# Kernel tuning notes

Measured on AMD Instinct MI355X. Metric: run time of the kernel, lower is better.

Reference implementation:

```python
import jax, jax.numpy as jnp
import numpy as np

B = 32768
NM = 3      # number of modalities (len(mk))
NE = 8      # number of experts
D_IN = 768
D_P = 128   # per-modality projection dim
D_X = D_P * NM  # 384, concatenated feature dim


def setup_inputs() -> dict:
    key = jax.random.key(0)
    ks = jax.random.split(key, 16)
    s = 0.02
    return {
        "feat_text": jax.random.normal(ks[0], (B, D_IN), jnp.float32),
        "feat_audio": jax.random.normal(ks[1], (B, D_IN), jnp.float32),
        "feat_video": jax.random.normal(ks[2], (B, D_IN), jnp.float32),
        "proj_w": jax.random.normal(ks[3], (NM, D_IN, D_P), jnp.float32) * s,
        "proj_b": jax.random.normal(ks[4], (NM, D_P), jnp.float32) * s,
        "exp_w1": jax.random.normal(ks[5], (NE, D_X, D_P), jnp.float32) * s,
        "exp_b1": jax.random.normal(ks[6], (NE, D_P), jnp.float32) * s,
        "exp_w2": jax.random.normal(ks[7], (NE, D_P, D_P), jnp.float32) * s,
        "exp_b2": jax.random.normal(ks[8], (NE, D_P), jnp.float32) * s,
        "gate_w": jax.random.normal(ks[9], (D_X, NE), jnp.float32) * s,
        "gate_b": jax.random.normal(ks[10], (NE,), jnp.float32) * s,
        "pre_w": jax.random.normal(ks[11], (D_P, 64), jnp.float32) * s,
        "pre_b": jax.random.normal(ks[12], (64,), jnp.float32) * s,
        "head_w": jax.random.normal(ks[13], (64, 2), jnp.float32) * s,
        "head_b": jax.random.normal(ks[14], (2,), jnp.float32) * s,
    }


def reference(feat_text, feat_audio, feat_video, proj_w, proj_b,
              exp_w1, exp_b1, exp_w2, exp_b2, gate_w, gate_b,
              pre_w, pre_b, head_w, head_b):
    feats = jnp.stack([feat_text, feat_audio, feat_video], axis=0)  # [M,B,768]
    # per-modality projections, then concat: [B, 128*M]
    proj = jnp.einsum('mbd,mdp->mbp', feats, proj_w) + proj_b[:, None, :]
    x = jnp.concatenate(jnp.split(proj, NM, axis=0), axis=-1)[0]  # [B, 384]
    # gate: softmax over 8 experts
    gw = jax.nn.softmax(x @ gate_w + gate_b, axis=-1)  # [B, 8]
    # all experts as batched GEMM: [E,B,128]
    h = jax.nn.relu(jnp.einsum('bx,exh->ebh', x, exp_w1) + exp_b1[:, None, :])
    eo = jnp.einsum('ebh,eho->ebo', h, exp_w2) + exp_b2[:, None, :]
    fused = jnp.einsum('be,ebh->bh', gw, eo)  # weighted sum over experts
    penult = jax.nn.relu(fused @ pre_w + pre_b)  # Dropout is identity in eval
    logits = penult @ head_w + head_b  # [B, 2]
    return logits
```

## Files before the change

### kernel.cpp

```cpp
#include <hip/hip_runtime.h>
#include <hip/hip_bf16.h>

#define B_ROWS 32768

typedef unsigned short u16;
typedef unsigned int u32;
typedef float f32x4 __attribute__((ext_vector_type(4)));
typedef __bf16 bf16x8 __attribute__((ext_vector_type(8)));

__device__ __forceinline__ u16 f2bf(float f){
    union { float f; u32 u; } v; v.f = f;
    return (u16)((v.u + 0x7FFFu + ((v.u >> 16) & 1u)) >> 16);
}
__device__ __forceinline__ float bf2f(u16 h){
    union { u32 u; float f; } v; v.u = ((u32)h) << 16; return v.f;
}
__device__ __forceinline__ u32 cvtpk(float lo, float hi){
    u32 r;
    asm("v_cvt_pk_bf16_f32 %0, %1, %2" : "=v"(r) : "v"(lo), "v"(hi));
    return r;
}
__device__ __forceinline__ void async_cp16(void* lds_dst, const void* g_src){
    __builtin_amdgcn_global_load_lds(
        (const __attribute__((address_space(1))) unsigned int*)g_src,
        (__attribute__((address_space(3))) unsigned int*)lds_dst, 16, 0, 0);
}

__global__ void cast_weights_kernel(const float* __restrict__ proj_w,
                                    const float* __restrict__ exp_w1,
                                    const float* __restrict__ exp_w2,
                                    const float* __restrict__ pre_w,
                                    const float* __restrict__ gate_w,
                                    u16* __restrict__ pimg, u16* __restrict__ w1img,
                                    u16* __restrict__ w2img, u16* __restrict__ prwT,
                                    u16* __restrict__ gwimg){
    int i = blockIdx.x * 256 + threadIdx.x;
    if (i < 294912){
        int m = i / 98304, r = i % 98304;
        int c = r / 4096, rr = r % 4096;
        int col = rr >> 5, kk = rr & 31;
        int kb = kk ^ (((col >> 1) & 3) << 3);
        pimg[i] = f2bf(proj_w[m*98304 + (c*32 + kb)*128 + col]);
    } else if (i < 688128){
        int j = i - 294912;
        int e = j / 49152, r = j % 49152;
        int ph = r / 4096, rr = r % 4096;
        int q = rr >> 10, col = (rr >> 3) & 127, el = rr & 7;
        w1img[j] = f2bf(exp_w1[e*49152 + (ph*32 + q*8 + el)*128 + col]);
    } else if (i < 819200){
        int j = i - 688128;
        int e = j / 16384, r = j % 16384;
        int c2 = r / 4096, rr = r % 4096;
        int q = rr >> 10, col = (rr >> 3) & 127, el = rr & 7;
        w2img[j] = f2bf(exp_w2[e*16384 + (c2*32 + q*8 + el)*128 + col]);
    } else if (i < 827392){
        int j = i - 819200;
        int o = j / 128, k = j % 128;
        prwT[j] = f2bf(pre_w[k*64 + o]);
    } else if (i < 833536){
        int j = i - 827392;
        int e = j / 384, k = j % 384;
        gwimg[j] = (e < 8) ? f2bf(gate_w[k*8 + e]) : (u16)0;
    }
}

#define XS_OFF   0
#define A_OFF    98304
#define B_OFF    147456
#define HS_OFF   98304
#define GWT_OFF  131072
#define B1_OFF   135168
#define B2_OFF   137216
#define WB_OFF   139264

__global__ __launch_bounds__(512, 2) void fused_kernel(
    const float* __restrict__ ft, const float* __restrict__ fa, const float* __restrict__ fv,
    const u16* __restrict__ pimg, const float* __restrict__ proj_b,
    const u16* __restrict__ w1img, const u16* __restrict__ w2img,
    const u16* __restrict__ prwT, const u16* __restrict__ gwimg,
    const float* __restrict__ gate_b, const float* __restrict__ exp_b1, const float* __restrict__ exp_b2,
    const float* __restrict__ pre_b, const float* __restrict__ head_w, const float* __restrict__ head_b,
    float* __restrict__ out)
{
    __shared__ __align__(16) char lds[163840];
    const int tid = threadIdx.x;
    const int lane = tid & 63, wid = tid >> 6;
    const int wr = wid >> 1, wc = wid & 1;
    const int lr = lane & 15, q = lane >> 4;
    const int blk = blockIdx.x;
    const int row0 = blk * 128;
    const char* w1b = (const char*)w1img;
    const char* w2b = (const char*)w2img;
    char* HsB = lds + HS_OFF;
    u16* b1L = (u16*)(lds + B1_OFF);
    u16* b2L = (u16*)(lds + B2_OFF);

    float pb0[4], pb1[4], pb2[4];
    #pragma unroll
    for (int ni = 0; ni < 4; ni++){
        int c = wc*64 + ni*16 + lr;
        pb0[ni] = proj_b[c];
        pb1[ni] = proj_b[128 + c];
        pb2[ni] = proj_b[256 + c];
    }
    asm volatile("s_waitcnt vmcnt(0)" ::: "memory");

    u32 aoffs[2];
    #pragma unroll
    for (int i = 0; i < 2; i++){
        int P = i*8192 + tid*16;
        int row = P >> 7, inner = P & 127;
        aoffs[i] = (u32)((row0 + row)*3072 + (inner ^ ((row & 7) << 4)));
    }

#define ASTAGE(c) do{                                                          \
        int mm_ = (c) / 24, kk_ = (c) % 24;                                    \
        const char* ab_ = (const char*)(mm_ == 0 ? ft : mm_ == 1 ? fa : fv);   \
        char* la_ = lds + A_OFF + ((c) % 3)*16384 + tid*16;                    \
        async_cp16(la_,        ab_ + aoffs[0] + kk_*128);                      \
        async_cp16(la_ + 8192, ab_ + aoffs[1] + kk_*128);                      \
    }while(0)

#define BSTAGE(c) do{                                                          \
        int mm_ = (c) / 24, kk_ = (c) % 24;                                    \
        async_cp16(lds + B_OFF + ((c) % 2)*8192 + tid*16,                      \
                   (const char*)pimg + mm_*196608 + kk_*8192 + tid*16);        \
    }while(0)

#define PCONSUME(c) do{                                                        \
        const char* Abuf = lds + A_OFF + ((c) % 3)*16384;                      \
        const char* Bbuf = lds + B_OFF + ((c) % 2)*8192;                       \
        bf16x8 af[2];                                                          \
        _Pragma("unroll")                                                      \
        for (int mi = 0; mi < 2; mi++){                                        \
            int row = wr*32 + mi*16 + lr;                                      \
            int aoff = row*128 + ((q*32) ^ ((row & 7) << 4));                  \
            f32x4 a0 = *(const f32x4*)(Abuf + aoff);                           \
            f32x4 a1 = *(const f32x4*)(Abuf + (aoff ^ 16));                    \
            union { u32 w[4]; bf16x8 v; } u;                                   \
            u.w[0] = cvtpk(a0.x, a0.y); u.w[1] = cvtpk(a0.z, a0.w);            \
            u.w[2] = cvtpk(a1.x, a1.y); u.w[3] = cvtpk(a1.z, a1.w);            \
            af[mi] = u.v;                                                      \
        }                                                                      \
        _Pragma("unroll")                                                      \
        for (int ni = 0; ni < 4; ni++){                                        \
            int col = wc*64 + ni*16 + lr;                                      \
            int boff = col*64 + ((q*16) ^ (((col >> 1) & 3) << 4));            \
            bf16x8 bf = *(const bf16x8*)(Bbuf + boff);                         \
            acc[0][ni] = __builtin_amdgcn_mfma_f32_16x16x32_bf16(af[0], bf, acc[0][ni], 0, 0, 0); \
            acc[1][ni] = __builtin_amdgcn_mfma_f32_16x16x32_bf16(af[1], bf, acc[1][ni], 0, 0, 0); \
        }                                                                      \
    }while(0)

#define PHASE_A_MOD(MC, PB) do{                                                \
        _Pragma("unroll 1")                                                    \
        for (int kt = 0; kt < 24; kt++){                                       \
            int t = MC*24 + kt;                                                \
            __builtin_amdgcn_sched_barrier(0);                                 \
            __builtin_amdgcn_s_barrier();                                      \
            if (t < 71) BSTAGE(t + 1);                                         \
            if (t < 70) ASTAGE(t + 2);                                         \
            if (t < 70)       asm volatile("s_waitcnt vmcnt(5)" ::: "memory"); \
            else if (t == 70) asm volatile("s_waitcnt vmcnt(3)" ::: "memory"); \
            else              asm volatile("s_waitcnt vmcnt(0)" ::: "memory"); \
            __builtin_amdgcn_s_barrier();                                      \
            __builtin_amdgcn_sched_barrier(0);                                 \
            PCONSUME(t);                                                       \
        }                                                                      \
        _Pragma("unroll")                                                      \
        for (int mi = 0; mi < 2; mi++)                                         \
            _Pragma("unroll")                                                  \
            for (int ni = 0; ni < 4; ni++){                                    \
                int lcol = wc*64 + ni*16 + lr;                                 \
                int colg = MC*128 + lcol;                                      \
                int ktI = colg >> 5, qI = (colg >> 3) & 3, el = colg & 7;      \
                _Pragma("unroll")                                              \
                for (int j = 0; j < 4; j++){                                   \
                    int row = wr*32 + mi*16 + q*4 + j;                         \
                    *(u16*)(lds + (row >> 6)*49152 + ktI*4096 + qI*1024        \
                            + (row & 63)*16 + el*2) = f2bf(acc[mi][ni][j] + PB[ni]); \
                    acc[mi][ni][j] = 0.f;                                      \
                }                                                              \
            }                                                                  \
    }while(0)

    f32x4 acc[2][4];
    #pragma unroll
    for (int i = 0; i < 2; i++)
        #pragma unroll
        for (int j = 0; j < 4; j++) acc[i][j] = {0.f, 0.f, 0.f, 0.f};

    BSTAGE(0); ASTAGE(0); ASTAGE(1);
    PHASE_A_MOD(0, pb0);
    PHASE_A_MOD(1, pb1);
    PHASE_A_MOD(2, pb2);
#undef ASTAGE
#undef BSTAGE
#undef PCONSUME
#undef PHASE_A_MOD

    asm volatile("s_waitcnt lgkmcnt(0)" ::: "memory");
    __builtin_amdgcn_sched_barrier(0);
    __builtin_amdgcn_s_barrier();

    {
        const char* src = w1b + tid*16;
        async_cp16(lds + WB_OFF + 0*8192 + tid*16, src);
        async_cp16(lds + WB_OFF + 1*8192 + tid*16, src + 8192);
        async_cp16(lds + WB_OFF + 2*8192 + tid*16, src + 16384);
    }
    for (int i = tid; i < 1024; i += 512){
        b1L[i] = f2bf(exp_b1[i]);
        b2L[i] = f2bf(exp_b2[i]);
    }
    {
        f32x4 ga = {0.f, 0.f, 0.f, 0.f};
        const char* xb = lds + (wid >> 2)*49152 + ((wid & 3)*16 + lr)*16 + q*1024;
        const u16* gwp = gwimg + lr*384 + q*8;
        #pragma unroll
        for (int kt = 0; kt < 12; kt++){
            bf16x8 af = *(const bf16x8*)(xb + kt*4096);
            bf16x8 gb = *(const bf16x8*)(gwp + kt*32);
            ga = __builtin_amdgcn_mfma_f32_16x16x32_bf16(af, gb, ga, 0, 0, 0);
        }
        float gbv = gate_b[lr & 7];
        float gw4[4];
        #pragma unroll
        for (int j = 0; j < 4; j++){
            float v = ga[j] + gbv;
            float mx = v;
            mx = fmaxf(mx, __shfl_xor(mx, 1));
            mx = fmaxf(mx, __shfl_xor(mx, 2));
            mx = fmaxf(mx, __shfl_xor(mx, 4));
            float s = __expf(v - mx);
            float t = s;
            t += __shfl_xor(t, 1);
            t += __shfl_xor(t, 2);
            t += __shfl_xor(t, 4);
            gw4[j] = s / t;
        }
        if (lr < 8){
            f32x4 wv = {gw4[0], gw4[1], gw4[2], gw4[3]};
            *(f32x4*)(lds + GWT_OFF + lr*512 + (wid*16 + q*4)*4) = wv;
        }
    }
    asm volatile("s_waitcnt vmcnt(0) lgkmcnt(0)" ::: "memory");
    __builtin_amdgcn_sched_barrier(0);
    __builtin_amdgcn_s_barrier();

#define WGROUP_STAGE(gg2) do{                                                  \
        int e2_ = (gg2) / 6, i2_ = (gg2) % 6;                                  \
        if (i2_ < 4){                                                          \
            const char* src_ = w1b + e2_*98304 + i2_*3*8192 + tid*16;          \
            async_cp16(lds + WB_OFF + 0*8192 + tid*16, src_);                  \
            async_cp16(lds + WB_OFF + 1*8192 + tid*16, src_ + 8192);           \
            async_cp16(lds + WB_OFF + 2*8192 + tid*16, src_ + 16384);          \
        } else {                                                               \
            const char* src_ = w2b + e2_*32768 + (i2_ - 4)*2*8192 + tid*16;    \
            async_cp16(lds + WB_OFF + 0*8192 + tid*16, src_);                  \
            async_cp16(lds + WB_OFF + 1*8192 + tid*16, src_ + 8192);           \
        }                                                                      \
    }while(0)

    f32x4 fus[2][4];
    #pragma unroll
    for (int i = 0; i < 2; i++)
        #pragma unroll
        for (int j = 0; j < 4; j++) fus[i][j] = {0.f, 0.f, 0.f, 0.f};

    #pragma unroll 1
    for (int e = 0; e < 8; e++){
        f32x4 ac1[2][4];
        #pragma unroll
        for (int i = 0; i < 2; i++)
            #pragma unroll
            for (int j = 0; j < 4; j++) ac1[i][j] = {0.f, 0.f, 0.f, 0.f};

        #pragma unroll 1
        for (int grp = 0; grp < 4; grp++){
            #pragma unroll
            for (int c = 0; c < 3; c++){
                int ph = grp*3 + c;
                const char* wsl = lds + WB_OFF + c*8192 + q*2048;
                const char* xa  = lds + (wr >> 1)*49152 + ph*4096 + q*1024;
                bf16x8 af0 = *(const bf16x8*)(xa + ((wr & 1)*32 + lr)*16);
                bf16x8 af1 = *(const bf16x8*)(xa + ((wr & 1)*32 + 16 + lr)*16);
                #pragma unroll
                for (int ni = 0; ni < 4; ni++){
                    bf16x8 bf = *(const bf16x8*)(wsl + (wc*64 + ni*16 + lr)*16);
                    ac1[0][ni] = __builtin_amdgcn_mfma_f32_16x16x32_bf16(af0, bf, ac1[0][ni], 0, 0, 0);
                    ac1[1][ni] = __builtin_amdgcn_mfma_f32_16x16x32_bf16(af1, bf, ac1[1][ni], 0, 0, 0);
                }
            }
            if (grp == 3){
                #pragma unroll
                for (int mi = 0; mi < 2; mi++)
                    #pragma unroll
                    for (int ni = 0; ni < 4; ni++){
                        int col = wc*64 + ni*16 + lr;
                        float b1v = bf2f(b1L[e*128 + col]);
                        #pragma unroll
                        for (int j = 0; j < 4; j++){
                            int row = wr*32 + mi*16 + q*4 + j;
                            *(u16*)(HsB + row*256 + ((col*2) ^ ((row & 7) << 4)))
                                = f2bf(fmaxf(ac1[mi][ni][j] + b1v, 0.f));
                        }
                    }
                asm volatile("s_waitcnt lgkmcnt(0)" ::: "memory");
            }
            __builtin_amdgcn_sched_barrier(0);
            __builtin_amdgcn_s_barrier();
            WGROUP_STAGE(e*6 + grp + 1);
            asm volatile("s_waitcnt vmcnt(0)" ::: "memory");
            __builtin_amdgcn_s_barrier();
            __builtin_amdgcn_sched_barrier(0);
        }

        f32x4 ac2[2][4];
        #pragma unroll
        for (int i = 0; i < 2; i++)
            #pragma unroll
            for (int j = 0; j < 4; j++) ac2[i][j] = {0.f, 0.f, 0.f, 0.f};

        #pragma unroll 1
        for (int grp = 0; grp < 2; grp++){
            #pragma unroll
            for (int c = 0; c < 2; c++){
                int p2 = grp*2 + c;
                const char* wsl = lds + WB_OFF + c*8192 + q*2048;
                int cb = p2*64 + q*16;
                int rowA = wr*32 + lr;
                int rowB = wr*32 + 16 + lr;
                bf16x8 af0 = *(const bf16x8*)(HsB + rowA*256 + (cb ^ ((rowA & 7) << 4)));
                bf16x8 af1 = *(const bf16x8*)(HsB + rowB*256 + (cb ^ ((rowB & 7) << 4)));
                #pragma unroll
                for (int ni = 0; ni < 4; ni++){
                    bf16x8 bf = *(const bf16x8*)(wsl + (wc*64 + ni*16 + lr)*16);
                    ac2[0][ni] = __builtin_amdgcn_mfma_f32_16x16x32_bf16(af0, bf, ac2[0][ni], 0, 0, 0);
                    ac2[1][ni] = __builtin_amdgcn_mfma_f32_16x16x32_bf16(af1, bf, ac2[1][ni], 0, 0, 0);
                }
            }
            int gg2 = e*6 + 5 + grp;
            __builtin_amdgcn_sched_barrier(0);
            __builtin_amdgcn_s_barrier();
            if (gg2 < 48){
                WGROUP_STAGE(gg2);
                asm volatile("s_waitcnt vmcnt(0)" ::: "memory");
            }
            __builtin_amdgcn_s_barrier();
            __builtin_amdgcn_sched_barrier(0);
        }
        #pragma unroll
        for (int mi = 0; mi < 2; mi++){
            f32x4 gwv = *(const f32x4*)(lds + GWT_OFF + e*512 + (wr*32 + mi*16 + q*4)*4);
            #pragma unroll
            for (int ni = 0; ni < 4; ni++){
                int col = wc*64 + ni*16 + lr;
                float b2v = bf2f(b2L[e*128 + col]);
                #pragma unroll
                for (int j = 0; j < 4; j++)
                    fus[mi][ni][j] += gwv[j] * (ac2[mi][ni][j] + b2v);
            }
        }
    }
#undef WGROUP_STAGE

    __builtin_amdgcn_sched_barrier(0);
    __builtin_amdgcn_s_barrier();
    #pragma unroll
    for (int mi = 0; mi < 2; mi++)
        #pragma unroll
        for (int ni = 0; ni < 4; ni++){
            int col = wc*64 + ni*16 + lr;
            #pragma unroll
            for (int j = 0; j < 4; j++){
                int row = wr*32 + mi*16 + q*4 + j;
                *(u16*)(HsB + row*256 + ((col*2) ^ ((row & 7) << 4))) = f2bf(fus[mi][ni][j]);
            }
        }
    asm volatile("s_waitcnt lgkmcnt(0)" ::: "memory");
    __builtin_amdgcn_sched_barrier(0);
    __builtin_amdgcn_s_barrier();

    f32x4 ap[4];
    #pragma unroll
    for (int i = 0; i < 4; i++) ap[i] = {0.f, 0.f, 0.f, 0.f};
    #pragma unroll
    for (int kt = 0; kt < 4; kt++){
        int row = wid*16 + lr;
        int cb = kt*64 + q*16;
        bf16x8 af = *(const bf16x8*)(HsB + row*256 + (cb ^ ((row & 7) << 4)));
        #pragma unroll
        for (int ni = 0; ni < 4; ni++){
            bf16x8 bf = *(const bf16x8*)(prwT + (size_t)(ni*16 + lr)*128 + kt*32 + q*8);
            ap[ni] = __builtin_amdgcn_mfma_f32_16x16x32_bf16(af, bf, ap[ni], 0, 0, 0);
        }
    }
    float* Pen = (float*)lds;
    #pragma unroll
    for (int ni = 0; ni < 4; ni++){
        int col = ni*16 + lr;
        float pbv = pre_b[col];
        #pragma unroll
        for (int j = 0; j < 4; j++){
            int row = wid*16 + q*4 + j;
            Pen[row*68 + col] = fmaxf(ap[ni][j] + pbv, 0.f);
        }
    }
    asm volatile("s_waitcnt lgkmcnt(0)" ::: "memory");
    __builtin_amdgcn_sched_barrier(0);
    __builtin_amdgcn_s_barrier();
    if (tid < 256){
        int r = tid >> 1, c = tid & 1;
        float s = head_b[c];
        #pragma unroll 8
        for (int k = 0; k < 64; k++) s += Pen[r*68 + k] * head_w[k*2 + c];
        out[(size_t)(blk*128 + r)*2 + c] = s;
    }
}

extern "C" void kernel_launch(void* const* d_in, const int* in_sizes, int n_in,
                              void* d_out, int out_size, void* d_ws, size_t ws_size,
                              hipStream_t stream) {
    const float* ft     = (const float*)d_in[0];
    const float* fa     = (const float*)d_in[1];
    const float* fv     = (const float*)d_in[2];
    const float* proj_w = (const float*)d_in[3];
    const float* proj_b = (const float*)d_in[4];
    const float* exp_w1 = (const float*)d_in[5];
    const float* exp_b1 = (const float*)d_in[6];
    const float* exp_w2 = (const float*)d_in[7];
    const float* exp_b2 = (const float*)d_in[8];
    const float* gate_w = (const float*)d_in[9];
    const float* gate_b = (const float*)d_in[10];
    const float* pre_w  = (const float*)d_in[11];
    const float* pre_b  = (const float*)d_in[12];
    const float* head_w = (const float*)d_in[13];
    const float* head_b = (const float*)d_in[14];
    float* out = (float*)d_out;

    u16* pimg  = (u16*)d_ws;
    u16* w1img = pimg + 294912;
    u16* w2img = w1img + 393216;
    u16* prwT  = w2img + 131072;
    u16* gwimg = prwT + 8192;

    cast_weights_kernel<<<3256, 256, 0, stream>>>(proj_w, exp_w1, exp_w2, pre_w, gate_w,
                                                  pimg, w1img, w2img, prwT, gwimg);
    fused_kernel<<<256, 512, 0, stream>>>(ft, fa, fv, pimg, proj_b,
                                          w1img, w2img, prwT, gwimg,
                                          gate_b, exp_b1, exp_b2,
                                          pre_b, head_w, head_b, out);
}
```

Before: 120.9 us.

## Halve workgroup to 4 waves, each wave computing a 64x64 tile

The fused kernel now runs 256 threads (4 waves) per block instead of 512. Each wave owns a 64-row by 64-column output tile with 4x4 MFMA accumulators instead of 2x4, and all staging loops, waitcnt counts and epilogues are rescaled to match. The goal is to reuse each B fragment across more MFMAs, cut LDS reads per flop and lower barrier overhead. In exchange it roughly doubles accumulator register pressure and halves the wave count that hides load latency, while the same 256 blocks and LDS footprint are kept.

After: 136.2 us. +12.7%, slower.

```diff
diff --git a/kernel.cpp b/kernel.cpp
--- a/kernel.cpp
+++ b/kernel.cpp
@@ -73,7 +73,7 @@
 #define B2_OFF   137216
 #define WB_OFF   139264
 
-__global__ __launch_bounds__(512, 2) void fused_kernel(
+__global__ __launch_bounds__(256, 1) void fused_kernel(
     const float* __restrict__ ft, const float* __restrict__ fa, const float* __restrict__ fv,
     const u16* __restrict__ pimg, const float* __restrict__ proj_b,
     const u16* __restrict__ w1img, const u16* __restrict__ w2img,
@@ -105,10 +105,10 @@
     }
     asm volatile("s_waitcnt vmcnt(0)" ::: "memory");
 
-    u32 aoffs[2];
-    #pragma unroll
-    for (int i = 0; i < 2; i++){
-        int P = i*8192 + tid*16;
+    u32 aoffs[4];
+    #pragma unroll
+    for (int i = 0; i < 4; i++){
+        int P = i*4096 + tid*16;
         int row = P >> 7, inner = P & 127;
         aoffs[i] = (u32)((row0 + row)*3072 + (inner ^ ((row & 7) << 4)));
     }
@@ -117,23 +117,27 @@
         int mm_ = (c) / 24, kk_ = (c) % 24;                                    \
         const char* ab_ = (const char*)(mm_ == 0 ? ft : mm_ == 1 ? fa : fv);   \
         char* la_ = lds + A_OFF + ((c) % 3)*16384 + tid*16;                    \
-        async_cp16(la_,        ab_ + aoffs[0] + kk_*128);                      \
-        async_cp16(la_ + 8192, ab_ + aoffs[1] + kk_*128);                      \
+        async_cp16(la_,         ab_ + aoffs[0] + kk_*128);                     \
+        async_cp16(la_ + 4096,  ab_ + aoffs[1] + kk_*128);                     \
+        async_cp16(la_ + 8192,  ab_ + aoffs[2] + kk_*128);                     \
+        async_cp16(la_ + 12288, ab_ + aoffs[3] + kk_*128);                     \
     }while(0)
 
 #define BSTAGE(c) do{                                                          \
         int mm_ = (c) / 24, kk_ = (c) % 24;                                    \
-        async_cp16(lds + B_OFF + ((c) % 2)*8192 + tid*16,                      \
-                   (const char*)pimg + mm_*196608 + kk_*8192 + tid*16);        \
+        const char* gb_ = (const char*)pimg + mm_*196608 + kk_*8192 + tid*16;  \
+        char* lb_ = lds + B_OFF + ((c) % 2)*8192 + tid*16;                     \
+        async_cp16(lb_,        gb_);                                           \
+        async_cp16(lb_ + 4096, gb_ + 4096);                                    \
     }while(0)
 
 #define PCONSUME(c) do{                                                        \
         const char* Abuf = lds + A_OFF + ((c) % 3)*16384;                      \
         const char* Bbuf = lds + B_OFF + ((c) % 2)*8192;                       \
-        bf16x8 af[2];                                                          \
+        bf16x8 af[4];                                                          \
         _Pragma("unroll")                                                      \
-        for (int mi = 0; mi < 2; mi++){                                        \
-            int row = wr*32 + mi*16 + lr;                                      \
+        for (int mi = 0; mi < 4; mi++){                                        \
+            int row = wr*64 + mi*16 + lr;                                      \
             int aoff = row*128 + ((q*32) ^ ((row & 7) << 4));                  \
             f32x4 a0 = *(const f32x4*)(Abuf + aoff);                           \
             f32x4 a1 = *(const f32x4*)(Abuf + (aoff ^ 16));                    \
@@ -147,8 +151,9 @@
             int col = wc*64 + ni*16 + lr;                                      \
             int boff = col*64 + ((q*16) ^ (((col >> 1) & 3) << 4));            \
             bf16x8 bf = *(const bf16x8*)(Bbuf + boff);                         \
-            acc[0][ni] = __builtin_amdgcn_mfma_f32_16x16x32_bf16(af[0], bf, acc[0][ni], 0, 0, 0); \
-            acc[1][ni] = __builtin_amdgcn_mfma_f32_16x16x32_bf16(af[1], bf, acc[1][ni], 0, 0, 0); \
+            _Pragma("unroll")                                                  \
+            for (int mi = 0; mi < 4; mi++)                                     \
+                acc[mi][ni] = __builtin_amdgcn_mfma_f32_16x16x32_bf16(af[mi], bf, acc[mi][ni], 0, 0, 0); \
         }                                                                      \
     }while(0)
 
@@ -160,15 +165,15 @@
             __builtin_amdgcn_s_barrier();                                      \
             if (t < 71) BSTAGE(t + 1);                                         \
             if (t < 70) ASTAGE(t + 2);                                         \
-            if (t < 70)       asm volatile("s_waitcnt vmcnt(5)" ::: "memory"); \
-            else if (t == 70) asm volatile("s_waitcnt vmcnt(3)" ::: "memory"); \
+            if (t < 70)       asm volatile("s_waitcnt vmcnt(10)" ::: "memory"); \
+            else if (t == 70) asm volatile("s_waitcnt vmcnt(6)" ::: "memory"); \
             else              asm volatile("s_waitcnt vmcnt(0)" ::: "memory"); \
             __builtin_amdgcn_s_barrier();                                      \
             __builtin_amdgcn_sched_barrier(0);                                 \
             PCONSUME(t);                                                       \
         }                                                                      \
         _Pragma("unroll")                                                      \
-        for (int mi = 0; mi < 2; mi++)                                         \
+        for (int mi = 0; mi < 4; mi++)                                         \
             _Pragma("unroll")                                                  \
             for (int ni = 0; ni < 4; ni++){                                    \
                 int lcol = wc*64 + ni*16 + lr;                                 \
@@ -176,7 +181,7 @@
                 int ktI = colg >> 5, qI = (colg >> 3) & 3, el = colg & 7;      \
                 _Pragma("unroll")                                              \
                 for (int j = 0; j < 4; j++){                                   \
-                    int row = wr*32 + mi*16 + q*4 + j;                         \
+                    int row = wr*64 + mi*16 + q*4 + j;                         \
                     *(u16*)(lds + (row >> 6)*49152 + ktI*4096 + qI*1024        \
                             + (row & 63)*16 + el*2) = f2bf(acc[mi][ni][j] + PB[ni]); \
                     acc[mi][ni][j] = 0.f;                                      \
@@ -184,9 +189,9 @@
             }                                                                  \
     }while(0)
 
-    f32x4 acc[2][4];
-    #pragma unroll
-    for (int i = 0; i < 2; i++)
+    f32x4 acc[4][4];
+    #pragma unroll
+    for (int i = 0; i < 4; i++)
         #pragma unroll
         for (int j = 0; j < 4; j++) acc[i][j] = {0.f, 0.f, 0.f, 0.f};
 
@@ -205,17 +210,21 @@
 
     {
         const char* src = w1b + tid*16;
-        async_cp16(lds + WB_OFF + 0*8192 + tid*16, src);
-        async_cp16(lds + WB_OFF + 1*8192 + tid*16, src + 8192);
-        async_cp16(lds + WB_OFF + 2*8192 + tid*16, src + 16384);
-    }
-    for (int i = tid; i < 1024; i += 512){
+        #pragma unroll
+        for (int s = 0; s < 3; s++){
+            async_cp16(lds + WB_OFF + s*8192 + tid*16,        src + s*8192);
+            async_cp16(lds + WB_OFF + s*8192 + tid*16 + 4096, src + s*8192 + 4096);
+        }
+    }
+    for (int i = tid; i < 1024; i += 256){
         b1L[i] = f2bf(exp_b1[i]);
         b2L[i] = f2bf(exp_b2[i]);
     }
-    {
+    #pragma unroll
+    for (int hr = 0; hr < 2; hr++){
+        int g16 = wid*2 + hr;
         f32x4 ga = {0.f, 0.f, 0.f, 0.f};
-        const char* xb = lds + (wid >> 2)*49152 + ((wid & 3)*16 + lr)*16 + q*1024;
+        const char* xb = lds + (g16 >> 2)*49152 + ((g16 & 3)*16 + lr)*16 + q*1024;
         const u16* gwp = gwimg + lr*384 + q*8;
         #pragma unroll
         for (int kt = 0; kt < 12; kt++){
@@ -241,7 +250,7 @@
         }
         if (lr < 8){
             f32x4 wv = {gw4[0], gw4[1], gw4[2], gw4[3]};
-            *(f32x4*)(lds + GWT_OFF + lr*512 + (wid*16 + q*4)*4) = wv;
+            *(f32x4*)(lds + GWT_OFF + lr*512 + (g16*16 + q*4)*4) = wv;
         }
     }
     asm volatile("s_waitcnt vmcnt(0) lgkmcnt(0)" ::: "memory");
@@ -251,28 +260,33 @@
 #define WGROUP_STAGE(gg2) do{                                                  \
         int e2_ = (gg2) / 6, i2_ = (gg2) % 6;                                  \
         if (i2_ < 4){                                                          \
-            const char* src_ = w1b + e2_*98304 + i2_*3*8192 + tid*16;          \
-            async_cp16(lds + WB_OFF + 0*8192 + tid*16, src_);                  \
-            async_cp16(lds + WB_OFF + 1*8192 + tid*16, src_ + 8192);           \
-            async_cp16(lds + WB_OFF + 2*8192 + tid*16, src_ + 16384);          \
+            const char* src_ = w1b + e2_*98304 + i2_*24576 + tid*16;           \
+            _Pragma("unroll")                                                  \
+            for (int s = 0; s < 3; s++){                                       \
+                async_cp16(lds + WB_OFF + s*8192 + tid*16,        src_ + s*8192);        \
+                async_cp16(lds + WB_OFF + s*8192 + tid*16 + 4096, src_ + s*8192 + 4096); \
+            }                                                                  \
         } else {                                                               \
-            const char* src_ = w2b + e2_*32768 + (i2_ - 4)*2*8192 + tid*16;    \
-            async_cp16(lds + WB_OFF + 0*8192 + tid*16, src_);                  \
-            async_cp16(lds + WB_OFF + 1*8192 + tid*16, src_ + 8192);           \
+            const char* src_ = w2b + e2_*32768 + (i2_ - 4)*16384 + tid*16;     \
+            _Pragma("unroll")                                                  \
+            for (int s = 0; s < 2; s++){                                       \
+                async_cp16(lds + WB_OFF + s*8192 + tid*16,        src_ + s*8192);        \
+                async_cp16(lds + WB_OFF + s*8192 + tid*16 + 4096, src_ + s*8192 + 4096); \
+            }                                                                  \
         }                                                                      \
     }while(0)
 
-    f32x4 fus[2][4];
-    #pragma unroll
-    for (int i = 0; i < 2; i++)
+    f32x4 fus[4][4];
+    #pragma unroll
+    for (int i = 0; i < 4; i++)
         #pragma unroll
         for (int j = 0; j < 4; j++) fus[i][j] = {0.f, 0.f, 0.f, 0.f};
 
     #pragma unroll 1
     for (int e = 0; e < 8; e++){
-        f32x4 ac1[2][4];
-        #pragma unroll
-        for (int i = 0; i < 2; i++)
+        f32x4 ac1[4][4];
+        #pragma unroll
+        for (int i = 0; i < 4; i++)
             #pragma unroll
             for (int j = 0; j < 4; j++) ac1[i][j] = {0.f, 0.f, 0.f, 0.f};
 
@@ -282,26 +296,29 @@
             for (int c = 0; c < 3; c++){
                 int ph = grp*3 + c;
                 const char* wsl = lds + WB_OFF + c*8192 + q*2048;
-                const char* xa  = lds + (wr >> 1)*49152 + ph*4096 + q*1024;
-                bf16x8 af0 = *(const bf16x8*)(xa + ((wr & 1)*32 + lr)*16);
-                bf16x8 af1 = *(const bf16x8*)(xa + ((wr & 1)*32 + 16 + lr)*16);
+                const char* xa  = lds + wr*49152 + ph*4096 + q*1024;
+                bf16x8 af[4];
+                #pragma unroll
+                for (int mi = 0; mi < 4; mi++)
+                    af[mi] = *(const bf16x8*)(xa + (mi*16 + lr)*16);
                 #pragma unroll
                 for (int ni = 0; ni < 4; ni++){
                     bf16x8 bf = *(const bf16x8*)(wsl + (wc*64 + ni*16 + lr)*16);
-                    ac1[0][ni] = __builtin_amdgcn_mfma_f32_16x16x32_bf16(af0, bf, ac1[0][ni], 0, 0, 0);
-                    ac1[1][ni] = __builtin_amdgcn_mfma_f32_16x16x32_bf16(af1, bf, ac1[1][ni], 0, 0, 0);
+                    #pragma unroll
+                    for (int mi = 0; mi < 4; mi++)
+                        ac1[mi][ni] = __builtin_amdgcn_mfma_f32_16x16x32_bf16(af[mi], bf, ac1[mi][ni], 0, 0, 0);
                 }
             }
             if (grp == 3){
                 #pragma unroll
-                for (int mi = 0; mi < 2; mi++)
+                for (int mi = 0; mi < 4; mi++)
                     #pragma unroll
                     for (int ni = 0; ni < 4; ni++){
                         int col = wc*64 + ni*16 + lr;
                         float b1v = bf2f(b1L[e*128 + col]);
                         #pragma unroll
                         for (int j = 0; j < 4; j++){
-                            int row = wr*32 + mi*16 + q*4 + j;
+                            int row = wr*64 + mi*16 + q*4 + j;
                             *(u16*)(HsB + row*256 + ((col*2) ^ ((row & 7) << 4)))
                                 = f2bf(fmaxf(ac1[mi][ni][j] + b1v, 0.f));
                         }
@@ -316,9 +333,9 @@
             __builtin_amdgcn_sched_barrier(0);
         }
 
-        f32x4 ac2[2][4];
-        #pragma unroll
-        for (int i = 0; i < 2; i++)
+        f32x4 ac2[4][4];
+        #pragma unroll
+        for (int i = 0; i < 4; i++)
             #pragma unroll
             for (int j = 0; j < 4; j++) ac2[i][j] = {0.f, 0.f, 0.f, 0.f};
 
@@ -329,15 +346,18 @@
                 int p2 = grp*2 + c;
                 const char* wsl = lds + WB_OFF + c*8192 + q*2048;
                 int cb = p2*64 + q*16;
-                int rowA = wr*32 + lr;
-                int rowB = wr*32 + 16 + lr;
-                bf16x8 af0 = *(const bf16x8*)(HsB + rowA*256 + (cb ^ ((rowA & 7) << 4)));
-                bf16x8 af1 = *(const bf16x8*)(HsB + rowB*256 + (cb ^ ((rowB & 7) << 4)));
+                bf16x8 af[4];
+                #pragma unroll
+                for (int mi = 0; mi < 4; mi++){
+                    int rowA = wr*64 + mi*16 + lr;
+                    af[mi] = *(const bf16x8*)(HsB + rowA*256 + (cb ^ ((rowA & 7) << 4)));
+                }
                 #pragma unroll
                 for (int ni = 0; ni < 4; ni++){
                     bf16x8 bf = *(const bf16x8*)(wsl + (wc*64 + ni*16 + lr)*16);
-                    ac2[0][ni] = __builtin_amdgcn_mfma_f32_16x16x32_bf16(af0, bf, ac2[0][ni], 0, 0, 0);
-                    ac2[1][ni] = __builtin_amdgcn_mfma_f32_16x16x32_bf16(af1, bf, ac2[1][ni], 0, 0, 0);
+                    #pragma unroll
+                    for (int mi = 0; mi < 4; mi++)
+                        ac2[mi][ni] = __builtin_amdgcn_mfma_f32_16x16x32_bf16(af[mi], bf, ac2[mi][ni], 0, 0, 0);
                 }
             }
             int gg2 = e*6 + 5 + grp;
@@ -351,8 +371,8 @@
             __builtin_amdgcn_sched_barrier(0);
         }
         #pragma unroll
-        for (int mi = 0; mi < 2; mi++){
-            f32x4 gwv = *(const f32x4*)(lds + GWT_OFF + e*512 + (wr*32 + mi*16 + q*4)*4);
+        for (int mi = 0; mi < 4; mi++){
+            f32x4 gwv = *(const f32x4*)(lds + GWT_OFF + e*512 + (wr*64 + mi*16 + q*4)*4);
             #pragma unroll
             for (int ni = 0; ni < 4; ni++){
                 int col = wc*64 + ni*16 + lr;
@@ -368,13 +388,13 @@
     __builtin_amdgcn_sched_barrier(0);
     __builtin_amdgcn_s_barrier();
     #pragma unroll
-    for (int mi = 0; mi < 2; mi++)
+    for (int mi = 0; mi < 4; mi++)
         #pragma unroll
         for (int ni = 0; ni < 4; ni++){
             int col = wc*64 + ni*16 + lr;
             #pragma unroll
             for (int j = 0; j < 4; j++){
-                int row = wr*32 + mi*16 + q*4 + j;
+                int row = wr*64 + mi*16 + q*4 + j;
                 *(u16*)(HsB + row*256 + ((col*2) ^ ((row & 7) << 4))) = f2bf(fus[mi][ni][j]);
             }
         }
@@ -382,35 +402,42 @@
     __builtin_amdgcn_sched_barrier(0);
     __builtin_amdgcn_s_barrier();
 
-    f32x4 ap[4];
-    #pragma unroll
-    for (int i = 0; i < 4; i++) ap[i] = {0.f, 0.f, 0.f, 0.f};
+    f32x4 ap[2][4];
+    #pragma unroll
+    for (int i = 0; i < 2; i++)
+        #pragma unroll
+        for (int j = 0; j < 4; j++) ap[i][j] = {0.f, 0.f, 0.f, 0.f};
     #pragma unroll
     for (int kt = 0; kt < 4; kt++){
-        int row = wid*16 + lr;
         int cb = kt*64 + q*16;
-        bf16x8 af = *(const bf16x8*)(HsB + row*256 + (cb ^ ((row & 7) << 4)));
+        #pragma unroll
+        for (int mi = 0; mi < 2; mi++){
+            int row = wid*32 + mi*16 + lr;
+            bf16x8 af = *(const bf16x8*)(HsB + row*256 + (cb ^ ((row & 7) << 4)));
+            #pragma unroll
+            for (int ni = 0; ni < 4; ni++){
+                bf16x8 bf = *(const bf16x8*)(prwT + (size_t)(ni*16 + lr)*128 + kt*32 + q*8);
+                ap[mi][ni] = __builtin_amdgcn_mfma_f32_16x16x32_bf16(af, bf, ap[mi][ni], 0, 0, 0);
+            }
+        }
+    }
+    float* Pen = (float*)lds;
+    #pragma unroll
+    for (int mi = 0; mi < 2; mi++)
         #pragma unroll
         for (int ni = 0; ni < 4; ni++){
-            bf16x8 bf = *(const bf16x8*)(prwT + (size_t)(ni*16 + lr)*128 + kt*32 + q*8);
-            ap[ni] = __builtin_amdgcn_mfma_f32_16x16x32_bf16(af, bf, ap[ni], 0, 0, 0);
-        }
-    }
-    float* Pen = (float*)lds;
-    #pragma unroll
-    for (int ni = 0; ni < 4; ni++){
-        int col = ni*16 + lr;
-        float pbv = pre_b[col];
-        #pragma unroll
-        for (int j = 0; j < 4; j++){
-            int row = wid*16 + q*4 + j;
-            Pen[row*68 + col] = fmaxf(ap[ni][j] + pbv, 0.f);
-        }
-    }
+            int col = ni*16 + lr;
+            float pbv = pre_b[col];
+            #pragma unroll
+            for (int j = 0; j < 4; j++){
+                int row = wid*32 + mi*16 + q*4 + j;
+                Pen[row*68 + col] = fmaxf(ap[mi][ni][j] + pbv, 0.f);
+            }
+        }
     asm volatile("s_waitcnt lgkmcnt(0)" ::: "memory");
     __builtin_amdgcn_sched_barrier(0);
     __builtin_amdgcn_s_barrier();
-    if (tid < 256){
+    {
         int r = tid >> 1, c = tid & 1;
         float s = head_b[c];
         #pragma unroll 8
@@ -447,7 +474,7 @@
 
     cast_weights_kernel<<<3256, 256, 0, stream>>>(proj_w, exp_w1, exp_w2, pre_w, gate_w,
                                                   pimg, w1img, w2img, prwT, gwimg);
-    fused_kernel<<<256, 512, 0, stream>>>(ft, fa, fv, pimg, proj_b,
+    fused_kernel<<<256, 256, 0, stream>>>(ft, fa, fv, pimg, proj_b,
                                           w1img, w2img, prwT, gwimg,
                                           gate_b, exp_b1, exp_b2,
                                           pre_b, head_w, head_b, out);
```
